# Kernel tuning notes

Measured on AMD Instinct MI355X. Metric: run time of the kernel, lower is better.

## Reference

```python
import jax, jax.numpy as jnp
import numpy as np

N_VERTS = 1_000_000
N_JOINTS = 55  # SMPL-X: NUM_JOINTS + 1


def setup_inputs() -> dict:
    key = jax.random.key(0)
    k1, k2, k3 = jax.random.split(key, 3)
    points = jax.random.normal(k1, (N_VERTS, 3), dtype=jnp.float32)
    w = jax.random.uniform(k2, (N_VERTS, N_JOINTS), dtype=jnp.float32)
    weights = w / jnp.sum(w, axis=-1, keepdims=True)  # LBS weights sum to 1 per vertex
    SE3 = jax.random.normal(k3, (N_JOINTS, 4, 4), dtype=jnp.float32)
    return {"points": points, "weights": weights, "SE3": SE3}


def reference(points, weights, SE3):
    # RigidTransform.weight: blend per-joint SE(3) matrices with per-vertex weights
    # weights: [N, J], SE3: [J, 4, 4] -> A: [N, 4, 4]
    A = jnp.einsum('nj,jkl->nkl', weights, SE3)
    R = A[:, :3, :3]  # [N, 3, 3]
    T = A[:, :3, 3]   # [N, 3]
    # RigidTransform._transform_points: R @ p + T
    return jnp.einsum('nkl,nl->nk', R, points) + T
```

## Files before the change

kernel.cpp:

```cpp
#include <hip/hip_runtime.h>

#define NJ  55
#define BLK 64
#define SLAB (BLK * NJ)

__global__ __launch_bounds__(BLK) void lbs_kernel(
    const float* __restrict__ points,
    const float* __restrict__ weights,
    const float* __restrict__ se3,
    float* __restrict__ out,
    int n_verts)
{
    __shared__ __align__(16) float s_w[SLAB];

    const int lane = threadIdx.x;
    const int row0 = blockIdx.x * BLK;

    if (row0 + BLK <= n_verts) {
        const float4* src = (const float4*)(weights + (size_t)row0 * NJ);
        float4* dst = (float4*)s_w;
        #pragma unroll
        for (int i = 0; i < SLAB / 4 / BLK; ++i)
            dst[lane + i * BLK] = src[lane + i * BLK];
        const int tail = SLAB / 4 - (SLAB / 4 / BLK) * BLK;
        if (lane < tail)
            dst[lane + (SLAB / 4 / BLK) * BLK] = src[lane + (SLAB / 4 / BLK) * BLK];
    } else {
        const int total = (n_verts - row0) * NJ;
        const float* src = weights + (size_t)row0 * NJ;
        for (int i = lane; i < total; i += BLK) s_w[i] = src[i];
    }
    __builtin_amdgcn_s_waitcnt(0);

    const int n = row0 + lane;
    if (n >= n_verts) return;

    float a[12];
    #pragma unroll
    for (int e = 0; e < 12; ++e) a[e] = 0.f;

    const float* wr = &s_w[lane * NJ];
    const float4* M = (const float4*)se3;

    #pragma unroll 5
    for (int j = 0; j < NJ; ++j) {
        const float w = wr[j];
        const float4 r0 = M[j * 4 + 0];
        const float4 r1 = M[j * 4 + 1];
        const float4 r2 = M[j * 4 + 2];
        a[0] += w * r0.x; a[1] += w * r0.y; a[2]  += w * r0.z; a[3]  += w * r0.w;
        a[4] += w * r1.x; a[5] += w * r1.y; a[6]  += w * r1.z; a[7]  += w * r1.w;
        a[8] += w * r2.x; a[9] += w * r2.y; a[10] += w * r2.z; a[11] += w * r2.w;
    }

    const float px = points[n * 3 + 0];
    const float py = points[n * 3 + 1];
    const float pz = points[n * 3 + 2];

    out[n * 3 + 0] = a[0] * px + a[1] * py + a[2]  * pz + a[3];
    out[n * 3 + 1] = a[4] * px + a[5] * py + a[6]  * pz + a[7];
    out[n * 3 + 2] = a[8] * px + a[9] * py + a[10] * pz + a[11];
}

extern "C" void kernel_launch(void* const* d_in, const int* in_sizes, int n_in,
                              void* d_out, int out_size, void* d_ws, size_t ws_size,
                              hipStream_t stream) {
    const float* points  = (const float*)d_in[0];
    const float* weights = (const float*)d_in[1];
    const float* se3     = (const float*)d_in[2];
    float* out = (float*)d_out;

    const int n_verts = in_sizes[0] / 3;
    const int grid = (n_verts + BLK - 1) / BLK;
    lbs_kernel<<<grid, BLK, 0, stream>>>(points, weights, se3, out, n_verts);
}
```

Measured before the change: 315.3 us.

## Use persistent blocks with double-buffered global_load_lds weight staging

Replaces the one-block-per-slab launch with a fixed grid of persistent blocks that walk slabs in a grid-stride loop. While one slab is computed, the next slab's weights are loaded straight into a second LDS buffer with global_load_lds, and vmcnt waits keep the load in flight during compute. The aim is to hide weight-load latency behind the blend math on this bandwidth-bound kernel. It doubles LDS per block, relies on a hand-written vmcnt literal that must match the number of issued loads, and handles leftover rows separately in block 0.

```diff
diff --git a/kernel.cpp b/kernel.cpp
--- a/kernel.cpp
+++ b/kernel.cpp
@@ -1,8 +1,33 @@
 #include <hip/hip_runtime.h>
 
-#define NJ  55
-#define BLK 64
-#define SLAB (BLK * NJ)
+#define NJ     55
+#define BLK    64
+#define SLABF  (BLK * NJ)
+#define SLABB  (SLABF * 4)
+#define NF16   13
+#define NF4    3
+#define NSTAGE (NF16 + NF4)
+#define GRID_BLOCKS 1280
+
+static_assert(NF16 * 1024 + NF4 * 256 == SLABB, "staging chunks must tile the slab exactly");
+static_assert(NSTAGE == 16, "vmcnt(16) literal below must equal NSTAGE");
+
+#define GLOAD_LDS(g, l, W)                                              \
+    __builtin_amdgcn_global_load_lds(                                   \
+        (const __attribute__((address_space(1))) void*)(g),             \
+        (__attribute__((address_space(3))) void*)(l), W, 0, 0)
+
+__device__ __forceinline__ void stage_slab(const float* __restrict__ gsrc,
+                                           float* lbase, int lane)
+{
+    #pragma unroll
+    for (int i = 0; i < NF16; ++i)
+        GLOAD_LDS(gsrc + i * 256 + lane * 4, lbase + i * 256, 16);
+    #pragma unroll
+    for (int k = 0; k < NF4; ++k)
+        GLOAD_LDS(gsrc + NF16 * 256 + k * 64 + lane,
+                  lbase + NF16 * 256 + k * 64, 4);
+}
 
 __global__ __launch_bounds__(BLK) void lbs_kernel(
     const float* __restrict__ points,
@@ -11,66 +36,95 @@
     float* __restrict__ out,
     int n_verts)
 {
-    __shared__ __align__(16) float s_w[SLAB];
+    __shared__ __align__(16) float s_w[2 * SLABF];
 
-    const int lane = threadIdx.x;
-    const int row0 = blockIdx.x * BLK;
+    const int lane   = threadIdx.x;
+    const int nslab  = n_verts / BLK;
+    const int stride = gridDim.x;
+    const float4* M  = (const float4*)se3;
 
-    if (row0 + BLK <= n_verts) {
-        const float4* src = (const float4*)(weights + (size_t)row0 * NJ);
-        float4* dst = (float4*)s_w;
-        #pragma unroll
-        for (int i = 0; i < SLAB / 4 / BLK; ++i)
-            dst[lane + i * BLK] = src[lane + i * BLK];
-        const int tail = SLAB / 4 - (SLAB / 4 / BLK) * BLK;
-        if (lane < tail)
-            dst[lane + (SLAB / 4 / BLK) * BLK] = src[lane + (SLAB / 4 / BLK) * BLK];
-    } else {
-        const int total = (n_verts - row0) * NJ;
-        const float* src = weights + (size_t)row0 * NJ;
-        for (int i = lane; i < total; i += BLK) s_w[i] = src[i];
-    }
-    __builtin_amdgcn_s_waitcnt(0);
+    int s = blockIdx.x;
+    if (s < nslab) {
+        stage_slab(weights + (size_t)s * SLABF, s_w, lane);
+        int cur = 0;
+        while (true) {
+            const int n = s * BLK + lane;
+            const float px = points[n * 3 + 0];
+            const float py = points[n * 3 + 1];
+            const float pz = points[n * 3 + 2];
+            __builtin_amdgcn_sched_barrier(0);
 
-    const int n = row0 + lane;
-    if (n >= n_verts) return;
+            const int snext = s + stride;
+            if (snext < nslab) {
+                stage_slab(weights + (size_t)snext * SLABF,
+                           s_w + (cur ^ 1) * SLABF, lane);
+                asm volatile("s_waitcnt vmcnt(16)" ::: "memory");
+            } else {
+                asm volatile("s_waitcnt vmcnt(0)" ::: "memory");
+            }
+            __builtin_amdgcn_sched_barrier(0);
 
-    float a[12];
-    #pragma unroll
-    for (int e = 0; e < 12; ++e) a[e] = 0.f;
+            const float* wr = s_w + cur * SLABF + lane * NJ;
+            float a[12];
+            #pragma unroll
+            for (int e = 0; e < 12; ++e) a[e] = 0.f;
+            #pragma unroll 5
+            for (int j = 0; j < NJ; ++j) {
+                const float w  = wr[j];
+                const float4 r0 = M[j * 4 + 0];
+                const float4 r1 = M[j * 4 + 1];
+                const float4 r2 = M[j * 4 + 2];
+                a[0] += w*r0.x; a[1] += w*r0.y; a[2]  += w*r0.z; a[3]  += w*r0.w;
+                a[4] += w*r1.x; a[5] += w*r1.y; a[6]  += w*r1.z; a[7]  += w*r1.w;
+                a[8] += w*r2.x; a[9] += w*r2.y; a[10] += w*r2.z; a[11] += w*r2.w;
+            }
+            out[n * 3 + 0] = a[0]*px + a[1]*py + a[2] *pz + a[3];
+            out[n * 3 + 1] = a[4]*px + a[5]*py + a[6] *pz + a[7];
+            out[n * 3 + 2] = a[8]*px + a[9]*py + a[10]*pz + a[11];
 
-    const float* wr = &s_w[lane * NJ];
-    const float4* M = (const float4*)se3;
-
-    #pragma unroll 5
-    for (int j = 0; j < NJ; ++j) {
-        const float w = wr[j];
-        const float4 r0 = M[j * 4 + 0];
-        const float4 r1 = M[j * 4 + 1];
-        const float4 r2 = M[j * 4 + 2];
-        a[0] += w * r0.x; a[1] += w * r0.y; a[2]  += w * r0.z; a[3]  += w * r0.w;
-        a[4] += w * r1.x; a[5] += w * r1.y; a[6]  += w * r1.z; a[7]  += w * r1.w;
-        a[8] += w * r2.x; a[9] += w * r2.y; a[10] += w * r2.z; a[11] += w * r2.w;
+            if (snext >= nslab) break;
+            s = snext;
+            cur ^= 1;
+        }
     }
 
-    const float px = points[n * 3 + 0];
-    const float py = points[n * 3 + 1];
-    const float pz = points[n * 3 + 2];
-
-    out[n * 3 + 0] = a[0] * px + a[1] * py + a[2]  * pz + a[3];
-    out[n * 3 + 1] = a[4] * px + a[5] * py + a[6]  * pz + a[7];
-    out[n * 3 + 2] = a[8] * px + a[9] * py + a[10] * pz + a[11];
+    const int rem = n_verts - nslab * BLK;
+    if (rem && blockIdx.x == 0 && lane < rem) {
+        const int n = nslab * BLK + lane;
+        const float* wr = weights + (size_t)n * NJ;
+        float a[12];
+        #pragma unroll
+        for (int e = 0; e < 12; ++e) a[e] = 0.f;
+        for (int j = 0; j < NJ; ++j) {
+            const float w  = wr[j];
+            const float4 r0 = M[j * 4 + 0];
+            const float4 r1 = M[j * 4 + 1];
+            const float4 r2 = M[j * 4 + 2];
+            a[0] += w*r0.x; a[1] += w*r0.y; a[2]  += w*r0.z; a[3]  += w*r0.w;
+            a[4] += w*r1.x; a[5] += w*r1.y; a[6]  += w*r1.z; a[7]  += w*r1.w;
+            a[8] += w*r2.x; a[9] += w*r2.y; a[10] += w*r2.z; a[11] += w*r2.w;
+        }
+        const float px = points[n * 3 + 0];
+        const float py = points[n * 3 + 1];
+        const float pz = points[n * 3 + 2];
+        out[n * 3 + 0] = a[0]*px + a[1]*py + a[2] *pz + a[3];
+        out[n * 3 + 1] = a[4]*px + a[5]*py + a[6] *pz + a[7];
+        out[n * 3 + 2] = a[8]*px + a[9]*py + a[10]*pz + a[11];
+    }
 }
 
 extern "C" void kernel_launch(void* const* d_in, const int* in_sizes, int n_in,
                               void* d_out, int out_size, void* d_ws, size_t ws_size,
-                              hipStream_t stream) {
+                              hipStream_t stream)
+{
     const float* points  = (const float*)d_in[0];
     const float* weights = (const float*)d_in[1];
     const float* se3     = (const float*)d_in[2];
     float* out = (float*)d_out;
 
     const int n_verts = in_sizes[0] / 3;
-    const int grid = (n_verts + BLK - 1) / BLK;
+    const int nslab   = n_verts / BLK;
+    int grid = GRID_BLOCKS;
+    if (grid > nslab) grid = (nslab > 0) ? nslab : 1;
     lbs_kernel<<<grid, BLK, 0, stream>>>(points, weights, se3, out, n_verts);
 }
```

After: 317.2 us. Within noise of the previous version (+0.6%).

## Load weight rows directly into registers instead of staging via LDS

Applied to the files above, without the earlier changes.

Removes the shared-memory staging of the weight slab and has each thread load its own 55-weight row into registers with vector loads, then fully unrolls the joint blend. The block size grows to 256 threads with a launch-bounds occupancy hint. The intent is to avoid the LDS round trip and barrier and to expose more memory-level parallelism. The risk is that per-thread strided row loads coalesce poorly across the wavefront and raise register pressure.

```diff
diff --git a/kernel.cpp b/kernel.cpp
--- a/kernel.cpp
+++ b/kernel.cpp
@@ -1,70 +1,72 @@
 #include <hip/hip_runtime.h>
 
 #define NJ  55
-#define BLK 64
-#define SLAB (BLK * NJ)
+#define BLK 256
 
-__global__ __launch_bounds__(BLK) void lbs_kernel(
+typedef float f4 __attribute__((ext_vector_type(4), aligned(4)));
+typedef float f2 __attribute__((ext_vector_type(2), aligned(4)));
+
+__global__ __launch_bounds__(BLK, 4) void lbs_kernel(
     const float* __restrict__ points,
     const float* __restrict__ weights,
     const float* __restrict__ se3,
     float* __restrict__ out,
     int n_verts)
 {
-    __shared__ __align__(16) float s_w[SLAB];
+    const int n = blockIdx.x * BLK + threadIdx.x;
+    if (n >= n_verts) return;
 
-    const int lane = threadIdx.x;
-    const int row0 = blockIdx.x * BLK;
+    const float* __restrict__ wrow = weights + (size_t)n * NJ;
 
-    if (row0 + BLK <= n_verts) {
-        const float4* src = (const float4*)(weights + (size_t)row0 * NJ);
-        float4* dst = (float4*)s_w;
-        #pragma unroll
-        for (int i = 0; i < SLAB / 4 / BLK; ++i)
-            dst[lane + i * BLK] = src[lane + i * BLK];
-        const int tail = SLAB / 4 - (SLAB / 4 / BLK) * BLK;
-        if (lane < tail)
-            dst[lane + (SLAB / 4 / BLK) * BLK] = src[lane + (SLAB / 4 / BLK) * BLK];
-    } else {
-        const int total = (n_verts - row0) * NJ;
-        const float* src = weights + (size_t)row0 * NJ;
-        for (int i = lane; i < total; i += BLK) s_w[i] = src[i];
-    }
-    __builtin_amdgcn_s_waitcnt(0);
+    f4 wv[13];
+    #pragma unroll
+    for (int i = 0; i < 13; ++i)
+        wv[i] = *(const f4*)(wrow + i * 4);
+    const f2    wt2 = *(const f2*)(wrow + 52);
+    const float wt1 = wrow[54];
 
-    const int n = row0 + lane;
-    if (n >= n_verts) return;
+    const float px = points[n * 3 + 0];
+    const float py = points[n * 3 + 1];
+    const float pz = points[n * 3 + 2];
+
+    const float4* __restrict__ M = (const float4*)se3;
 
     float a[12];
     #pragma unroll
     for (int e = 0; e < 12; ++e) a[e] = 0.f;
 
-    const float* wr = &s_w[lane * NJ];
-    const float4* M = (const float4*)se3;
+    #define LBS_STEP(J, W)                                                  \
+        do {                                                                \
+            const float w_ = (W);                                           \
+            const float4 r0 = M[(J) * 4 + 0];                               \
+            const float4 r1 = M[(J) * 4 + 1];                               \
+            const float4 r2 = M[(J) * 4 + 2];                               \
+            a[0] += w_*r0.x; a[1] += w_*r0.y; a[2]  += w_*r0.z; a[3]  += w_*r0.w; \
+            a[4] += w_*r1.x; a[5] += w_*r1.y; a[6]  += w_*r1.z; a[7]  += w_*r1.w; \
+            a[8] += w_*r2.x; a[9] += w_*r2.y; a[10] += w_*r2.z; a[11] += w_*r2.w; \
+        } while (0)
 
-    #pragma unroll 5
-    for (int j = 0; j < NJ; ++j) {
-        const float w = wr[j];
-        const float4 r0 = M[j * 4 + 0];
-        const float4 r1 = M[j * 4 + 1];
-        const float4 r2 = M[j * 4 + 2];
-        a[0] += w * r0.x; a[1] += w * r0.y; a[2]  += w * r0.z; a[3]  += w * r0.w;
-        a[4] += w * r1.x; a[5] += w * r1.y; a[6]  += w * r1.z; a[7]  += w * r1.w;
-        a[8] += w * r2.x; a[9] += w * r2.y; a[10] += w * r2.z; a[11] += w * r2.w;
+    #pragma unroll
+    for (int i = 0; i < 13; ++i) {
+        LBS_STEP(i * 4 + 0, wv[i].x);
+        LBS_STEP(i * 4 + 1, wv[i].y);
+        LBS_STEP(i * 4 + 2, wv[i].z);
+        LBS_STEP(i * 4 + 3, wv[i].w);
     }
+    LBS_STEP(52, wt2.x);
+    LBS_STEP(53, wt2.y);
+    LBS_STEP(54, wt1);
+    #undef LBS_STEP
 
-    const float px = points[n * 3 + 0];
-    const float py = points[n * 3 + 1];
-    const float pz = points[n * 3 + 2];
-
-    out[n * 3 + 0] = a[0] * px + a[1] * py + a[2]  * pz + a[3];
-    out[n * 3 + 1] = a[4] * px + a[5] * py + a[6]  * pz + a[7];
-    out[n * 3 + 2] = a[8] * px + a[9] * py + a[10] * pz + a[11];
+    out[n * 3 + 0] = a[0]*px + a[1]*py + a[2] *pz + a[3];
+    out[n * 3 + 1] = a[4]*px + a[5]*py + a[6] *pz + a[7];
+    out[n * 3 + 2] = a[8]*px + a[9]*py + a[10]*pz + a[11];
 }
 
 extern "C" void kernel_launch(void* const* d_in, const int* in_sizes, int n_in,
                               void* d_out, int out_size, void* d_ws, size_t ws_size,
-                              hipStream_t stream) {
+                              hipStream_t stream)
+{
     const float* points  = (const float*)d_in[0];
     const float* weights = (const float*)d_in[1];
     const float* se3     = (const float*)d_in[2];
```

Measured after the change: 321.4 us. About the same (+2.0%).
